# Optimization experiments

Hardware: AMD Instinct MI355X
Metric: run time of the kernel (lower is better)

The kernel has to match this reference:

```python
import jax, jax.numpy as jnp
import numpy as np
import math

D_MODEL = 2048
NUM_HEADS = 16
QUERY_GROUPS = 4
HEAD_DIM = D_MODEL // NUM_HEADS  # 128
B, T = 2, 2048


def setup_inputs() -> dict:
    key = jax.random.key(0)
    ks = jax.random.split(key, 9)
    s = 0.02
    return {
        "x": jax.random.normal(ks[0], (B, T, D_MODEL), dtype=jnp.float32),
        "Wq": jax.random.normal(ks[1], (D_MODEL, NUM_HEADS * HEAD_DIM), dtype=jnp.float32) * s,
        "bq": jnp.zeros((NUM_HEADS * HEAD_DIM,), dtype=jnp.float32),
        "Wk": jax.random.normal(ks[2], (D_MODEL, QUERY_GROUPS * HEAD_DIM), dtype=jnp.float32) * s,
        "bk": jnp.zeros((QUERY_GROUPS * HEAD_DIM,), dtype=jnp.float32),
        "Wv": jax.random.normal(ks[3], (D_MODEL, QUERY_GROUPS * HEAD_DIM), dtype=jnp.float32) * s,
        "bv": jnp.zeros((QUERY_GROUPS * HEAD_DIM,), dtype=jnp.float32),
        "Wo": jax.random.normal(ks[4], (D_MODEL, D_MODEL), dtype=jnp.float32) * s,
        "bo": jnp.zeros((D_MODEL,), dtype=jnp.float32),
    }


def reference(x, Wq, bq, Wk, bk, Wv, bv, Wo, bo):
    Bb, Tt, Dd = x.shape
    G, H, hd = QUERY_GROUPS, NUM_HEADS, HEAD_DIM
    m = H // G  # heads per group
    # projections
    q = (x @ Wq + bq).reshape(Bb, Tt, G, m, hd)   # [B,T,G,m,hd]
    k = (x @ Wk + bk).reshape(Bb, Tt, G, hd)      # [B,T,G,hd]
    v = (x @ Wv + bv).reshape(Bb, Tt, G, hd)
    # scores with native group broadcast (no explicit K/V expansion)
    scores = jnp.einsum('btgmd,bsgd->bgmts', q, k) / math.sqrt(hd)  # [B,G,m,T,T]
    p = jax.nn.softmax(scores, axis=-1)
    out = jnp.einsum('bgmts,bsgd->btgmd', p, v).reshape(Bb, Tt, Dd)
    # output projection (dropout is identity in eval / p=0)
    return out @ Wo + bo
```

## Files before the change

### kernel.cpp

```cpp
#include <hip/hip_runtime.h>

#define D_MODEL 2048
#define T_SEQ   2048
#define NBATCH  2
#define NH      16
#define NG      4
#define HD      128
#define NQKV    3072

typedef short bf16x8 __attribute__((ext_vector_type(8)));
typedef float f32x4  __attribute__((ext_vector_type(4)));
typedef short s16x4  __attribute__((ext_vector_type(4)));

__device__ __forceinline__ short f2bf(float f) {
  union { float f; unsigned u; } v; v.f = f;
  unsigned r = v.u + 0x7fffu + ((v.u >> 16) & 1u);
  return (short)(r >> 16);
}

__device__ __forceinline__ float bf2f(short s) {
  union { unsigned u; float f; } v; v.u = ((unsigned)(unsigned short)s) << 16;
  return v.f;
}

__device__ __forceinline__ float fast_exp2(float x) {
#if __has_builtin(__builtin_amdgcn_exp2f)
  return __builtin_amdgcn_exp2f(x);
#else
  return __expf(x * 0.6931471805599453f);
#endif
}

__device__ __forceinline__ void gload16(const void* g, void* l) {
  __builtin_amdgcn_global_load_lds(
      (const __attribute__((address_space(1))) void*)g,
      (__attribute__((address_space(3))) void*)l, 16, 0, 0);
}

__global__ __launch_bounds__(256) void convert_x_kernel(
    const float* __restrict__ x, short* __restrict__ o, int n) {
  int i = (blockIdx.x * 256 + threadIdx.x) * 4;
  if (i >= n) return;
  float4 v = *(const float4*)(x + i);
  s16x4 s;
  s[0] = f2bf(v.x); s[1] = f2bf(v.y); s[2] = f2bf(v.z); s[3] = f2bf(v.w);
  *(s16x4*)(o + i) = s;
}

__global__ __launch_bounds__(256) void wtrans_kernel(
    const float* __restrict__ W, short* __restrict__ dst,
    int K, int N, int rowOff, int dstStride) {
  __shared__ float t[32][33];
  int tx = threadIdx.x & 31, ty = threadIdx.x >> 5;
  int kb = blockIdx.x * 32, nb = blockIdx.y * 32;
#pragma unroll
  for (int i = 0; i < 4; ++i)
    t[ty + 8*i][tx] = W[(long)(kb + ty + 8*i) * N + nb + tx];
  __syncthreads();
#pragma unroll
  for (int i = 0; i < 4; ++i)
    dst[(long)(rowOff + nb + ty + 8*i) * dstStride + kb + tx] = f2bf(t[tx][ty + 8*i]);
}

__global__ __launch_bounds__(256) void vtrans_kernel(
    const short* __restrict__ qkv, short* __restrict__ vt) {
  __shared__ short t[32][33];
  int bg = blockIdx.z; int b = bg >> 2, g = bg & 3;
  int sb = blockIdx.x * 32, db = blockIdx.y * 32;
  int tx = threadIdx.x & 31, ty = threadIdx.x >> 5;
  const short* src = qkv + (long)(b * T_SEQ) * NQKV + D_MODEL + NG * HD + g * HD;
#pragma unroll
  for (int i = 0; i < 4; ++i)
    t[ty + 8*i][tx] = src[(long)(sb + ty + 8*i) * NQKV + db + tx];
  __syncthreads();
  short* dst = vt + ((long)bg * HD + db) * T_SEQ + sb;
#pragma unroll
  for (int i = 0; i < 4; ++i)
    dst[(long)(ty + 8*i) * T_SEQ + tx] = t[tx][ty + 8*i];
}

__global__ __launch_bounds__(256) void gemm_kernel(
    const short* __restrict__ A, const short* __restrict__ BT,
    const float* __restrict__ b0, const float* __restrict__ b1, const float* __restrict__ b2,
    void* __restrict__ Cout, int M, int N, int K, int mode) {
  __shared__ __align__(16) short As[128 * 32];
  __shared__ __align__(16) short Bs[128 * 32];
  const int tid = threadIdx.x;
  const int w = tid >> 6, lane = tid & 63;
  const int l15 = lane & 15, quad = lane >> 4;
  const int wr = w & 1, wc = w >> 1;
  const int nb = blockIdx.x, mb = blockIdx.y;
  const short* Ab = A + (long)mb * 128 * K;
  const short* Bb = BT + (long)nb * 128 * K;

  f32x4 acc[4][4];
#pragma unroll
  for (int i = 0; i < 4; ++i)
#pragma unroll
    for (int j = 0; j < 4; ++j) acc[i][j] = 0.0f;

  for (int k0 = 0; k0 < K; k0 += 32) {
    __syncthreads();
#pragma unroll
    for (int t = 0; t < 2; ++t) {
      int chunk = w * 128 + t * 64 + lane;
      int r = chunk >> 2, c = chunk & 3;
      int gc = c ^ ((r >> 1) & 3);
      gload16(Ab + (long)r * K + k0 + gc * 8, As + (w * 128 + t * 64) * 8);
      gload16(Bb + (long)r * K + k0 + gc * 8, Bs + (w * 128 + t * 64) * 8);
    }
    __syncthreads();
    bf16x8 af[4], bfr[4];
#pragma unroll
    for (int i = 0; i < 4; ++i) {
      int r = wr * 64 + i * 16 + l15;
      af[i] = *(const bf16x8*)(As + r * 32 + ((quad ^ ((r >> 1) & 3)) * 8));
    }
#pragma unroll
    for (int j = 0; j < 4; ++j) {
      int r = wc * 64 + j * 16 + l15;
      bfr[j] = *(const bf16x8*)(Bs + r * 32 + ((quad ^ ((r >> 1) & 3)) * 8));
    }
#pragma unroll
    for (int i = 0; i < 4; ++i)
#pragma unroll
      for (int j = 0; j < 4; ++j)
        acc[i][j] = __builtin_amdgcn_mfma_f32_16x16x32_bf16(af[i], bfr[j], acc[i][j], 0, 0, 0);
  }

  float biasv[4];
#pragma unroll
  for (int j = 0; j < 4; ++j) {
    int col = nb * 128 + wc * 64 + j * 16 + l15;
    float bv;
    if (mode == 0) {
      if (col < 2048)      bv = b0[col];
      else if (col < 2560) bv = b1[col - 2048];
      else                 bv = b2[col - 2560];
    } else bv = b0[col];
    biasv[j] = bv;
  }
  if (mode == 0) {
    short* C = (short*)Cout;
#pragma unroll
    for (int i = 0; i < 4; ++i)
#pragma unroll
      for (int j = 0; j < 4; ++j)
#pragma unroll
        for (int r = 0; r < 4; ++r) {
          int row = mb * 128 + wr * 64 + i * 16 + quad * 4 + r;
          int col = nb * 128 + wc * 64 + j * 16 + l15;
          C[(long)row * N + col] = f2bf(acc[i][j][r] + biasv[j]);
        }
  } else {
    float* C = (float*)Cout;
#pragma unroll
    for (int i = 0; i < 4; ++i)
#pragma unroll
      for (int j = 0; j < 4; ++j)
#pragma unroll
        for (int r = 0; r < 4; ++r) {
          int row = mb * 128 + wr * 64 + i * 16 + quad * 4 + r;
          int col = nb * 128 + wc * 64 + j * 16 + l15;
          C[(long)row * N + col] = acc[i][j][r] + biasv[j];
        }
  }
}

__global__ __launch_bounds__(256, 4) void attn_kernel(
    const short* __restrict__ qkv, const short* __restrict__ vt,
    short* __restrict__ aout) {
  __shared__ __align__(16) short Ks[64 * 128];
  __shared__ __align__(16) short Vs[128 * 64];
  __shared__ __align__(16) short Ps[64 * 64];
  const int tid = threadIdx.x;
  const int w = tid >> 6, lane = tid & 63;
  const int l15 = lane & 15, quad = lane >> 4;
  const int qt = blockIdx.x, h = blockIdx.y, b = blockIdx.z;
  const int g = h >> 2;
  const short* qbase = qkv + (long)(b * T_SEQ + qt * 64) * NQKV + h * HD;
  const short* kbase = qkv + (long)(b * T_SEQ) * NQKV + D_MODEL + g * HD;
  const short* vbase = vt + (long)(b * NG + g) * HD * T_SEQ;
  const float QSCALE = 0.08838834764831845f * 1.4426950408889634f;

  const int qrow = w * 16 + l15;

#pragma unroll
  for (int t = 0; t < 4; ++t) {
    int chunk = w * 256 + t * 64 + lane;
    int r = chunk >> 4, c = chunk & 15;
    int gc = c ^ (r & 15);
    gload16(qbase + (long)r * NQKV + gc * 8, Ks + (w * 256 + t * 64) * 8);
  }
  __syncthreads();
  bf16x8 qfrag[4];
#pragma unroll
  for (int ks = 0; ks < 4; ++ks) {
    bf16x8 v = *(const bf16x8*)(Ks + qrow * 128 + (((ks * 4 + quad) ^ (qrow & 15)) * 8));
#pragma unroll
    for (int e = 0; e < 8; ++e) v[e] = f2bf(bf2f(v[e]) * QSCALE);
    qfrag[ks] = v;
  }

  bf16x8 ones;
#pragma unroll
  for (int e = 0; e < 8; ++e) ones[e] = (short)0x3F80;

  f32x4 lacc = 0.0f;
  f32x4 oacc[8];
#pragma unroll
  for (int j = 0; j < 8; ++j) oacc[j] = 0.0f;

  for (int st = 0; st < T_SEQ / 64; ++st) {
    const int s0 = st * 64;
    __syncthreads();
    const short* kb = kbase + (long)s0 * NQKV;
#pragma unroll
    for (int t = 0; t < 4; ++t) {
      int chunk = w * 256 + t * 64 + lane;
      int r = chunk >> 4, c = chunk & 15;
      int gc = c ^ (r & 15);
      gload16(kb + (long)r * NQKV + gc * 8, Ks + (w * 256 + t * 64) * 8);
    }
    const short* vb = vbase + s0;
#pragma unroll
    for (int t = 0; t < 4; ++t) {
      int chunk = w * 256 + t * 64 + lane;
      int r = chunk >> 3, c = chunk & 7;
      int gc = c ^ (r & 7);
      gload16(vb + (long)r * T_SEQ + gc * 8, Vs + (w * 256 + t * 64) * 8);
    }
    __syncthreads();

    f32x4 sacc[4];
#pragma unroll
    for (int j = 0; j < 4; ++j) sacc[j] = 0.0f;
#pragma unroll
    for (int ks = 0; ks < 4; ++ks) {
#pragma unroll
      for (int j = 0; j < 4; ++j) {
        int krow = j * 16 + l15;
        bf16x8 bfr = *(const bf16x8*)(Ks + krow * 128 + (((ks * 4 + quad) ^ (krow & 15)) * 8));
        sacc[j] = __builtin_amdgcn_mfma_f32_16x16x32_bf16(qfrag[ks], bfr, sacc[j], 0, 0, 0);
      }
    }

#pragma unroll
    for (int j = 0; j < 4; ++j)
#pragma unroll
      for (int r = 0; r < 4; ++r) {
        short pb = f2bf(fast_exp2(sacc[j][r]));
        int row = w * 16 + quad * 4 + r;
        int col = j * 16 + l15;
        Ps[row * 64 + (((col >> 3) ^ (row & 7)) * 8) + (col & 7)] = pb;
      }

#pragma unroll
    for (int ks = 0; ks < 2; ++ks) {
      bf16x8 af = *(const bf16x8*)(Ps + qrow * 64 + (((ks * 4 + quad) ^ (qrow & 7)) * 8));
      lacc = __builtin_amdgcn_mfma_f32_16x16x32_bf16(af, ones, lacc, 0, 0, 0);
#pragma unroll
      for (int j = 0; j < 8; ++j) {
        int vrow = j * 16 + l15;
        bf16x8 bfr = *(const bf16x8*)(Vs + vrow * 64 + (((ks * 4 + quad) ^ (vrow & 7)) * 8));
        oacc[j] = __builtin_amdgcn_mfma_f32_16x16x32_bf16(af, bfr, oacc[j], 0, 0, 0);
      }
    }
  }

  float inv[4];
#pragma unroll
  for (int r = 0; r < 4; ++r) inv[r] = 1.0f / lacc[r];
  short* obase = aout + (long)(b * T_SEQ + qt * 64) * D_MODEL + h * HD;
#pragma unroll
  for (int j = 0; j < 8; ++j)
#pragma unroll
    for (int r = 0; r < 4; ++r) {
      int row = w * 16 + quad * 4 + r;
      int col = j * 16 + l15;
      obase[(long)row * D_MODEL + col] = f2bf(oacc[j][r] * inv[r]);
    }
}

extern "C" void kernel_launch(void* const* d_in, const int* in_sizes, int n_in,
                              void* d_out, int out_size, void* d_ws, size_t ws_size,
                              hipStream_t stream) {
  const float* x  = (const float*)d_in[0];
  const float* Wq = (const float*)d_in[1];
  const float* bq = (const float*)d_in[2];
  const float* Wk = (const float*)d_in[3];
  const float* bk = (const float*)d_in[4];
  const float* Wv = (const float*)d_in[5];
  const float* bv = (const float*)d_in[6];
  const float* Wo = (const float*)d_in[7];
  const float* bo = (const float*)d_in[8];

  const long NTOK = (long)NBATCH * T_SEQ;
  short* xb    = (short*)d_ws;
  short* wqkvT = xb + NTOK * D_MODEL;
  short* woT   = wqkvT + (long)NQKV * D_MODEL;
  short* qkvb  = woT + (long)D_MODEL * D_MODEL;
  short* vtb   = qkvb + NTOK * NQKV;
  short* attnb = vtb + (long)NBATCH * NG * HD * T_SEQ;

  int nX = (int)(NTOK * D_MODEL);
  convert_x_kernel<<<nX / (256 * 4), 256, 0, stream>>>(x, xb, nX);
  wtrans_kernel<<<dim3(D_MODEL / 32, D_MODEL / 32), 256, 0, stream>>>(Wq, wqkvT, D_MODEL, D_MODEL, 0, D_MODEL);
  wtrans_kernel<<<dim3(D_MODEL / 32, 512 / 32), 256, 0, stream>>>(Wk, wqkvT, D_MODEL, 512, 2048, D_MODEL);
  wtrans_kernel<<<dim3(D_MODEL / 32, 512 / 32), 256, 0, stream>>>(Wv, wqkvT, D_MODEL, 512, 2560, D_MODEL);
  wtrans_kernel<<<dim3(D_MODEL / 32, D_MODEL / 32), 256, 0, stream>>>(Wo, woT, D_MODEL, D_MODEL, 0, D_MODEL);

  gemm_kernel<<<dim3(NQKV / 128, NTOK / 128), 256, 0, stream>>>(
      xb, wqkvT, bq, bk, bv, (void*)qkvb, (int)NTOK, NQKV, D_MODEL, 0);

  vtrans_kernel<<<dim3(T_SEQ / 32, HD / 32, NBATCH * NG), 256, 0, stream>>>(qkvb, vtb);

  attn_kernel<<<dim3(T_SEQ / 64, NH, NBATCH), 256, 0, stream>>>(qkvb, vtb, attnb);

  gemm_kernel<<<dim3(D_MODEL / 128, NTOK / 128), 256, 0, stream>>>(
      attnb, woT, bo, bo, bo, (void*)d_out, (int)NTOK, D_MODEL, D_MODEL, 1);
}
```

Before: 359.6 us.

## Use 32x32x16 MFMA and split KV tile across waves in attention

```diff
diff --git a/kernel.cpp b/kernel.cpp
--- a/kernel.cpp
+++ b/kernel.cpp
@@ -10,6 +10,7 @@
 
 typedef short bf16x8 __attribute__((ext_vector_type(8)));
 typedef float f32x4  __attribute__((ext_vector_type(4)));
+typedef float f32x16 __attribute__((ext_vector_type(16)));
 typedef short s16x4  __attribute__((ext_vector_type(4)));
 
 __device__ __forceinline__ short f2bf(float f) {
@@ -167,15 +168,18 @@
   }
 }
 
-__global__ __launch_bounds__(256, 4) void attn_kernel(
+__global__ __launch_bounds__(256, 3) void attn_kernel(
     const short* __restrict__ qkv, const short* __restrict__ vt,
     short* __restrict__ aout) {
-  __shared__ __align__(16) short Ks[64 * 128];
-  __shared__ __align__(16) short Vs[128 * 64];
-  __shared__ __align__(16) short Ps[64 * 64];
+  __shared__ __align__(16) short smem[64 * 128 + 128 * 64 + 64 * 64];
+  short* Ks = smem;
+  short* Vs = smem + 64 * 128;
+  short* Ps = smem + 64 * 128 + 128 * 64;
+
   const int tid = threadIdx.x;
   const int w = tid >> 6, lane = tid & 63;
-  const int l15 = lane & 15, quad = lane >> 4;
+  const int l31 = lane & 31, hi = lane >> 5;
+  const int wr = w & 1, wc = w >> 1;
   const int qt = blockIdx.x, h = blockIdx.y, b = blockIdx.z;
   const int g = h >> 2;
   const short* qbase = qkv + (long)(b * T_SEQ + qt * 64) * NQKV + h * HD;
@@ -183,8 +187,6 @@
   const short* vbase = vt + (long)(b * NG + g) * HD * T_SEQ;
   const float QSCALE = 0.08838834764831845f * 1.4426950408889634f;
 
-  const int qrow = w * 16 + l15;
-
 #pragma unroll
   for (int t = 0; t < 4; ++t) {
     int chunk = w * 256 + t * 64 + lane;
@@ -193,10 +195,12 @@
     gload16(qbase + (long)r * NQKV + gc * 8, Ks + (w * 256 + t * 64) * 8);
   }
   __syncthreads();
-  bf16x8 qfrag[4];
-#pragma unroll
-  for (int ks = 0; ks < 4; ++ks) {
-    bf16x8 v = *(const bf16x8*)(Ks + qrow * 128 + (((ks * 4 + quad) ^ (qrow & 15)) * 8));
+  const int qr = wr * 32 + l31;
+  bf16x8 qfrag[8];
+#pragma unroll
+  for (int ks = 0; ks < 8; ++ks) {
+    int ch = 2 * ks + hi;
+    bf16x8 v = *(const bf16x8*)(Ks + qr * 128 + ((ch ^ (qr & 15)) * 8));
 #pragma unroll
     for (int e = 0; e < 8; ++e) v[e] = f2bf(bf2f(v[e]) * QSCALE);
     qfrag[ks] = v;
@@ -206,10 +210,13 @@
 #pragma unroll
   for (int e = 0; e < 8; ++e) ones[e] = (short)0x3F80;
 
-  f32x4 lacc = 0.0f;
-  f32x4 oacc[8];
-#pragma unroll
-  for (int j = 0; j < 8; ++j) oacc[j] = 0.0f;
+  f32x16 lacc = 0.0f;
+  f32x16 oacc[4];
+#pragma unroll
+  for (int dt = 0; dt < 4; ++dt) oacc[dt] = 0.0f;
+
+  short* myPs = Ps + w * 1024;
+  const int kr = wc * 32 + l31;
 
   for (int st = 0; st < T_SEQ / 64; ++st) {
     const int s0 = st * 64;
@@ -232,54 +239,80 @@
     }
     __syncthreads();
 
-    f32x4 sacc[4];
-#pragma unroll
-    for (int j = 0; j < 4; ++j) sacc[j] = 0.0f;
-#pragma unroll
-    for (int ks = 0; ks < 4; ++ks) {
-#pragma unroll
-      for (int j = 0; j < 4; ++j) {
-        int krow = j * 16 + l15;
-        bf16x8 bfr = *(const bf16x8*)(Ks + krow * 128 + (((ks * 4 + quad) ^ (krow & 15)) * 8));
-        sacc[j] = __builtin_amdgcn_mfma_f32_16x16x32_bf16(qfrag[ks], bfr, sacc[j], 0, 0, 0);
+    f32x16 sacc = 0.0f;
+#pragma unroll
+    for (int ks = 0; ks < 8; ++ks) {
+      int ch = 2 * ks + hi;
+      bf16x8 bfr = *(const bf16x8*)(Ks + kr * 128 + ((ch ^ (kr & 15)) * 8));
+      sacc = __builtin_amdgcn_mfma_f32_32x32x16_bf16(qfrag[ks], bfr, sacc, 0, 0, 0);
+    }
+
+#pragma unroll
+    for (int reg = 0; reg < 16; ++reg) {
+      short pb = f2bf(fast_exp2(sacc[reg]));
+      int row = (reg & 3) + 8 * (reg >> 2) + 4 * hi;
+      int col = l31;
+      int ch = col >> 3;
+      myPs[row * 32 + ((ch ^ (row & 3)) * 8) + (col & 7)] = pb;
+    }
+
+    bf16x8 pfrag[2];
+#pragma unroll
+    for (int k2 = 0; k2 < 2; ++k2) {
+      int ch = 2 * k2 + hi;
+      pfrag[k2] = *(const bf16x8*)(myPs + l31 * 32 + ((ch ^ (l31 & 3)) * 8));
+    }
+    lacc = __builtin_amdgcn_mfma_f32_32x32x16_bf16(pfrag[0], ones, lacc, 0, 0, 0);
+    lacc = __builtin_amdgcn_mfma_f32_32x32x16_bf16(pfrag[1], ones, lacc, 0, 0, 0);
+#pragma unroll
+    for (int dt = 0; dt < 4; ++dt)
+#pragma unroll
+      for (int k2 = 0; k2 < 2; ++k2) {
+        int d = dt * 32 + l31;
+        int ch = wc * 4 + 2 * k2 + hi;
+        bf16x8 bfr = *(const bf16x8*)(Vs + d * 64 + ((ch ^ (d & 7)) * 8));
+        oacc[dt] = __builtin_amdgcn_mfma_f32_32x32x16_bf16(pfrag[k2], bfr, oacc[dt], 0, 0, 0);
       }
-    }
-
-#pragma unroll
-    for (int j = 0; j < 4; ++j)
-#pragma unroll
-      for (int r = 0; r < 4; ++r) {
-        short pb = f2bf(fast_exp2(sacc[j][r]));
-        int row = w * 16 + quad * 4 + r;
-        int col = j * 16 + l15;
-        Ps[row * 64 + (((col >> 3) ^ (row & 7)) * 8) + (col & 7)] = pb;
+  }
+
+  __syncthreads();
+  float* Os = (float*)smem;
+  float* Ls = (float*)(smem + 64 * 128 + 128 * 64);
+  if (wc == 1) {
+#pragma unroll
+    for (int dt = 0; dt < 4; ++dt)
+#pragma unroll
+      for (int reg = 0; reg < 16; ++reg) {
+        int row = wr * 32 + (reg & 3) + 8 * (reg >> 2) + 4 * hi;
+        Os[row * 128 + dt * 32 + l31] = oacc[dt][reg];
       }
-
-#pragma unroll
-    for (int ks = 0; ks < 2; ++ks) {
-      bf16x8 af = *(const bf16x8*)(Ps + qrow * 64 + (((ks * 4 + quad) ^ (qrow & 7)) * 8));
-      lacc = __builtin_amdgcn_mfma_f32_16x16x32_bf16(af, ones, lacc, 0, 0, 0);
-#pragma unroll
-      for (int j = 0; j < 8; ++j) {
-        int vrow = j * 16 + l15;
-        bf16x8 bfr = *(const bf16x8*)(Vs + vrow * 64 + (((ks * 4 + quad) ^ (vrow & 7)) * 8));
-        oacc[j] = __builtin_amdgcn_mfma_f32_16x16x32_bf16(af, bfr, oacc[j], 0, 0, 0);
+    if (l31 == 0) {
+#pragma unroll
+      for (int reg = 0; reg < 16; ++reg) {
+        int row = wr * 32 + (reg & 3) + 8 * (reg >> 2) + 4 * hi;
+        Ls[row] = lacc[reg];
       }
     }
   }
-
-  float inv[4];
-#pragma unroll
-  for (int r = 0; r < 4; ++r) inv[r] = 1.0f / lacc[r];
-  short* obase = aout + (long)(b * T_SEQ + qt * 64) * D_MODEL + h * HD;
-#pragma unroll
-  for (int j = 0; j < 8; ++j)
-#pragma unroll
-    for (int r = 0; r < 4; ++r) {
-      int row = w * 16 + quad * 4 + r;
-      int col = j * 16 + l15;
-      obase[(long)row * D_MODEL + col] = f2bf(oacc[j][r] * inv[r]);
-    }
+  __syncthreads();
+  if (wc == 0) {
+    short* obase = aout + (long)(b * T_SEQ + qt * 64) * D_MODEL + h * HD;
+    float inv[16];
+#pragma unroll
+    for (int reg = 0; reg < 16; ++reg) {
+      int row = wr * 32 + (reg & 3) + 8 * (reg >> 2) + 4 * hi;
+      inv[reg] = 1.0f / (lacc[reg] + Ls[row]);
+    }
+#pragma unroll
+    for (int dt = 0; dt < 4; ++dt)
+#pragma unroll
+      for (int reg = 0; reg < 16; ++reg) {
+        int row = wr * 32 + (reg & 3) + 8 * (reg >> 2) + 4 * hi;
+        int col = dt * 32 + l31;
+        float o = oacc[dt][reg] + Os[row * 128 + col];
+        obase[(long)row * D_MODEL + col] = f2bf(o * inv[reg]);
+      }
+  }
 }
 
 extern "C" void kernel_launch(void* const* d_in, const int* in_sizes, int n_in,
```

New measurement: 394.2 us. 9.6% more time.

## Process 128 query rows per attention block to reuse K/V tiles

Applied to the files above, without the earlier changes.

```diff
diff --git a/kernel.cpp b/kernel.cpp
--- a/kernel.cpp
+++ b/kernel.cpp
@@ -167,49 +167,55 @@
   }
 }
 
-__global__ __launch_bounds__(256, 4) void attn_kernel(
+__global__ __launch_bounds__(256, 3) void attn_kernel(
     const short* __restrict__ qkv, const short* __restrict__ vt,
     short* __restrict__ aout) {
-  __shared__ __align__(16) short Ks[64 * 128];
-  __shared__ __align__(16) short Vs[128 * 64];
-  __shared__ __align__(16) short Ps[64 * 64];
+  __shared__ __align__(16) short smem[24576];
+  short* Ks = smem;
+  short* Vs = smem + 8192;
+  short* Ps = smem + 16384;
+
   const int tid = threadIdx.x;
   const int w = tid >> 6, lane = tid & 63;
   const int l15 = lane & 15, quad = lane >> 4;
   const int qt = blockIdx.x, h = blockIdx.y, b = blockIdx.z;
   const int g = h >> 2;
-  const short* qbase = qkv + (long)(b * T_SEQ + qt * 64) * NQKV + h * HD;
+  const short* qbase = qkv + (long)(b * T_SEQ + qt * 128) * NQKV + h * HD;
   const short* kbase = qkv + (long)(b * T_SEQ) * NQKV + D_MODEL + g * HD;
   const short* vbase = vt + (long)(b * NG + g) * HD * T_SEQ;
   const float QSCALE = 0.08838834764831845f * 1.4426950408889634f;
 
-  const int qrow = w * 16 + l15;
-
-#pragma unroll
-  for (int t = 0; t < 4; ++t) {
-    int chunk = w * 256 + t * 64 + lane;
+#pragma unroll
+  for (int t = 0; t < 8; ++t) {
+    int chunk = w * 512 + t * 64 + lane;
     int r = chunk >> 4, c = chunk & 15;
     int gc = c ^ (r & 15);
-    gload16(qbase + (long)r * NQKV + gc * 8, Ks + (w * 256 + t * 64) * 8);
+    gload16(qbase + (long)r * NQKV + gc * 8, smem + (w * 512 + t * 64) * 8);
   }
   __syncthreads();
-  bf16x8 qfrag[4];
-#pragma unroll
-  for (int ks = 0; ks < 4; ++ks) {
-    bf16x8 v = *(const bf16x8*)(Ks + qrow * 128 + (((ks * 4 + quad) ^ (qrow & 15)) * 8));
-#pragma unroll
-    for (int e = 0; e < 8; ++e) v[e] = f2bf(bf2f(v[e]) * QSCALE);
-    qfrag[ks] = v;
+  bf16x8 qfrag[2][4];
+#pragma unroll
+  for (int set = 0; set < 2; ++set) {
+    int qr = w * 32 + set * 16 + l15;
+#pragma unroll
+    for (int ks = 0; ks < 4; ++ks) {
+      bf16x8 v = *(const bf16x8*)(smem + qr * 128 + (((ks * 4 + quad) ^ (qr & 15)) * 8));
+#pragma unroll
+      for (int e = 0; e < 8; ++e) v[e] = f2bf(bf2f(v[e]) * QSCALE);
+      qfrag[set][ks] = v;
+    }
   }
 
   bf16x8 ones;
 #pragma unroll
   for (int e = 0; e < 8; ++e) ones[e] = (short)0x3F80;
 
-  f32x4 lacc = 0.0f;
-  f32x4 oacc[8];
-#pragma unroll
-  for (int j = 0; j < 8; ++j) oacc[j] = 0.0f;
+  f32x4 lacc[2] = {f32x4(0.0f), f32x4(0.0f)};
+  f32x4 oacc[2][8];
+#pragma unroll
+  for (int set = 0; set < 2; ++set)
+#pragma unroll
+    for (int j = 0; j < 8; ++j) oacc[set][j] = 0.0f;
 
   for (int st = 0; st < T_SEQ / 64; ++st) {
     const int s0 = st * 64;
@@ -232,54 +238,63 @@
     }
     __syncthreads();
 
-    f32x4 sacc[4];
-#pragma unroll
-    for (int j = 0; j < 4; ++j) sacc[j] = 0.0f;
-#pragma unroll
-    for (int ks = 0; ks < 4; ++ks) {
-#pragma unroll
-      for (int j = 0; j < 4; ++j) {
-        int krow = j * 16 + l15;
-        bf16x8 bfr = *(const bf16x8*)(Ks + krow * 128 + (((ks * 4 + quad) ^ (krow & 15)) * 8));
-        sacc[j] = __builtin_amdgcn_mfma_f32_16x16x32_bf16(qfrag[ks], bfr, sacc[j], 0, 0, 0);
+#pragma unroll
+    for (int set = 0; set < 2; ++set) {
+      f32x4 sacc[4];
+#pragma unroll
+      for (int j = 0; j < 4; ++j) sacc[j] = 0.0f;
+#pragma unroll
+      for (int ks = 0; ks < 4; ++ks) {
+#pragma unroll
+        for (int j = 0; j < 4; ++j) {
+          int krow = j * 16 + l15;
+          bf16x8 bfr = *(const bf16x8*)(Ks + krow * 128 + (((ks * 4 + quad) ^ (krow & 15)) * 8));
+          sacc[j] = __builtin_amdgcn_mfma_f32_16x16x32_bf16(qfrag[set][ks], bfr, sacc[j], 0, 0, 0);
+        }
       }
-    }
-
-#pragma unroll
-    for (int j = 0; j < 4; ++j)
-#pragma unroll
-      for (int r = 0; r < 4; ++r) {
-        short pb = f2bf(fast_exp2(sacc[j][r]));
-        int row = w * 16 + quad * 4 + r;
-        int col = j * 16 + l15;
-        Ps[row * 64 + (((col >> 3) ^ (row & 7)) * 8) + (col & 7)] = pb;
-      }
-
+#pragma unroll
+      for (int j = 0; j < 4; ++j)
+#pragma unroll
+        for (int r = 0; r < 4; ++r) {
+          short pb = f2bf(fast_exp2(sacc[j][r]));
+          int row = w * 32 + set * 16 + quad * 4 + r;
+          int col = j * 16 + l15;
+          Ps[row * 64 + (((col >> 3) ^ (row & 7)) * 8) + (col & 7)] = pb;
+        }
+    }
+
+    const int qr0 = w * 32 + l15, qr1 = w * 32 + 16 + l15;
 #pragma unroll
     for (int ks = 0; ks < 2; ++ks) {
-      bf16x8 af = *(const bf16x8*)(Ps + qrow * 64 + (((ks * 4 + quad) ^ (qrow & 7)) * 8));
-      lacc = __builtin_amdgcn_mfma_f32_16x16x32_bf16(af, ones, lacc, 0, 0, 0);
+      bf16x8 af0 = *(const bf16x8*)(Ps + qr0 * 64 + (((ks * 4 + quad) ^ (qr0 & 7)) * 8));
+      bf16x8 af1 = *(const bf16x8*)(Ps + qr1 * 64 + (((ks * 4 + quad) ^ (qr1 & 7)) * 8));
+      lacc[0] = __builtin_amdgcn_mfma_f32_16x16x32_bf16(af0, ones, lacc[0], 0, 0, 0);
+      lacc[1] = __builtin_amdgcn_mfma_f32_16x16x32_bf16(af1, ones, lacc[1], 0, 0, 0);
 #pragma unroll
       for (int j = 0; j < 8; ++j) {
         int vrow = j * 16 + l15;
         bf16x8 bfr = *(const bf16x8*)(Vs + vrow * 64 + (((ks * 4 + quad) ^ (vrow & 7)) * 8));
-        oacc[j] = __builtin_amdgcn_mfma_f32_16x16x32_bf16(af, bfr, oacc[j], 0, 0, 0);
+        oacc[0][j] = __builtin_amdgcn_mfma_f32_16x16x32_bf16(af0, bfr, oacc[0][j], 0, 0, 0);
+        oacc[1][j] = __builtin_amdgcn_mfma_f32_16x16x32_bf16(af1, bfr, oacc[1][j], 0, 0, 0);
       }
     }
   }
 
-  float inv[4];
-#pragma unroll
-  for (int r = 0; r < 4; ++r) inv[r] = 1.0f / lacc[r];
-  short* obase = aout + (long)(b * T_SEQ + qt * 64) * D_MODEL + h * HD;
-#pragma unroll
-  for (int j = 0; j < 8; ++j)
-#pragma unroll
-    for (int r = 0; r < 4; ++r) {
-      int row = w * 16 + quad * 4 + r;
-      int col = j * 16 + l15;
-      obase[(long)row * D_MODEL + col] = f2bf(oacc[j][r] * inv[r]);
-    }
+  short* obase = aout + (long)(b * T_SEQ + qt * 128) * D_MODEL + h * HD;
+#pragma unroll
+  for (int set = 0; set < 2; ++set) {
+    float inv[4];
+#pragma unroll
+    for (int r = 0; r < 4; ++r) inv[r] = 1.0f / lacc[set][r];
+#pragma unroll
+    for (int j = 0; j < 8; ++j)
+#pragma unroll
+      for (int r = 0; r < 4; ++r) {
+        int row = w * 32 + set * 16 + quad * 4 + r;
+        int col = j * 16 + l15;
+        obase[(long)row * D_MODEL + col] = f2bf(oacc[set][j][r] * inv[r]);
+      }
+  }
 }
 
 extern "C" void kernel_launch(void* const* d_in, const int* in_sizes, int n_in,
@@ -315,7 +330,7 @@
 
   vtrans_kernel<<<dim3(T_SEQ / 32, HD / 32, NBATCH * NG), 256, 0, stream>>>(qkvb, vtb);
 
-  attn_kernel<<<dim3(T_SEQ / 64, NH, NBATCH), 256, 0, stream>>>(qkvb, vtb, attnb);
+  attn_kernel<<<dim3(T_SEQ / 128, NH, NBATCH), 256, 0, stream>>>(qkvb, vtb, attnb);
 
   gemm_kernel<<<dim3(D_MODEL / 128, NTOK / 128), 256, 0, stream>>>(
       attnb, woT, bo, bo, bo, (void*)d_out, (int)NTOK, D_MODEL, D_MODEL, 1);
```

New measurement: 418.6 us. 1.16x slower.
